# Optimization experiments

Measured on AMD Instinct MI355X. Metric: run time of the kernel, lower is better.

Reference implementation:

```python
import jax, jax.numpy as jnp
import numpy as np

B, N, D_SIM = 4096, 64, 768
NLI_DIM = 768
KK = 5
H1, NUM_CLASSES = 1024, 4


def setup_inputs() -> dict:
    key = jax.random.key(0)
    ks = jax.random.split(key, 8)
    sim_stance_emb = jax.random.normal(ks[0], (B, D_SIM), dtype=jnp.float32)
    nli_stance_emb = jax.random.normal(ks[1], (B, NLI_DIM), dtype=jnp.float32)
    sim_body_emb = jax.random.normal(ks[2], (B, N, D_SIM), dtype=jnp.float32)
    nli_body_emb = jax.random.normal(ks[3], (B, N, NLI_DIM), dtype=jnp.float32)
    fan1 = (KK + 1) * NLI_DIM
    W1 = jax.random.uniform(ks[4], (H1, fan1), jnp.float32, -1.0, 1.0) / jnp.sqrt(fan1)
    b1 = jax.random.uniform(ks[5], (H1,), jnp.float32, -1.0, 1.0) / jnp.sqrt(fan1)
    W2 = jax.random.uniform(ks[6], (NUM_CLASSES, H1), jnp.float32, -1.0, 1.0) / jnp.sqrt(H1)
    b2 = jax.random.uniform(ks[7], (NUM_CLASSES,), jnp.float32, -1.0, 1.0) / jnp.sqrt(H1)
    return {"sim_stance_emb": sim_stance_emb, "nli_stance_emb": nli_stance_emb,
            "sim_body_emb": sim_body_emb, "nli_body_emb": nli_body_emb,
            "W1": W1, "b1": b1, "W2": W2, "b2": b2}


def reference(sim_stance_emb, nli_stance_emb, sim_body_emb, nli_body_emb, W1, b1, W2, b2):
    # sims[b, n] = <sim_stance_emb[b], sim_body_emb[b, n]>  (bmm + squeeze)
    sims = jnp.einsum('bd,bnd->bn', sim_stance_emb, sim_body_emb)
    _, top_idx = jax.lax.top_k(sims, KK)                      # [B, KK]
    # gather top-k nli body sentence embeddings: [B, KK, NLI_DIM]
    top_emb = jnp.take_along_axis(nli_body_emb, top_idx[:, :, None], axis=1)
    xx = jnp.concatenate([nli_stance_emb, top_emb.reshape(top_emb.shape[0], -1)], axis=1)
    xx = jax.nn.relu(xx @ W1.T + b1)
    return xx @ W2.T + b2
```

## Files before the change

### kernel.cpp

```cpp
#include <hip/hip_runtime.h>
#include <stdint.h>
#include <stddef.h>

#define B_N   4096
#define NSENT 64
#define DDIM  768
#define TOPK  5
#define FAN1  4608
#define H1DIM 1024
#define NCLS  4
#define KDIM  4608

typedef __attribute__((ext_vector_type(8))) __bf16 bf16x8;
typedef __attribute__((ext_vector_type(4))) float  f32x4;

__device__ __forceinline__ unsigned short f2bf(float f) {
    unsigned int u = __float_as_uint(f);
    unsigned int r = (u + 0x7fffu + ((u >> 16) & 1u)) >> 16;
    return (unsigned short)r;
}

__device__ __forceinline__ void gl_lds16(const void* g, void* l) {
    __builtin_amdgcn_global_load_lds((__attribute__((address_space(1))) void*)(g),
                                     (__attribute__((address_space(3))) void*)(l),
                                     16, 0, 0);
}

__global__ __launch_bounds__(256) void k_topk_gather(
    const float* __restrict__ sim_stance,
    const float* __restrict__ sim_body,
    const float* __restrict__ nli_stance,
    const float* __restrict__ nli_body,
    unsigned short* __restrict__ xx)
{
    const int b    = blockIdx.x;
    const int tid  = threadIdx.x;
    const int lane = tid & 63;
    const int wave = tid >> 6;
    __shared__ float sims[NSENT];
    __shared__ int   topidx[TOPK];

    const float4* st4 = (const float4*)(sim_stance + (size_t)b * DDIM);
    const float4  s0 = st4[lane], s1 = st4[64 + lane], s2 = st4[128 + lane];

    const float* bodyb = sim_body + (size_t)b * NSENT * DDIM;
    for (int n = wave; n < NSENT; n += 4) {
        const float4* r4 = (const float4*)(bodyb + (size_t)n * DDIM);
        float4 a = r4[lane], c = r4[64 + lane], e = r4[128 + lane];
        float p = a.x*s0.x + a.y*s0.y + a.z*s0.z + a.w*s0.w
                + c.x*s1.x + c.y*s1.y + c.z*s1.z + c.w*s1.w
                + e.x*s2.x + e.y*s2.y + e.z*s2.z + e.w*s2.w;
        #pragma unroll
        for (int off = 32; off; off >>= 1) p += __shfl_xor(p, off);
        if (lane == 0) sims[n] = p;
    }
    __syncthreads();

    if (wave == 0) {
        float v = sims[lane];
        #pragma unroll
        for (int k = 0; k < TOPK; ++k) {
            float bv = v; int bi = lane;
            #pragma unroll
            for (int off = 32; off; off >>= 1) {
                float ov = __shfl_xor(bv, off);
                int   oi = __shfl_xor(bi, off);
                if (ov > bv || (ov == bv && oi < bi)) { bv = ov; bi = oi; }
            }
            if (lane == 0) topidx[k] = bi;
            if (lane == bi) v = -3.402823466e38f;
        }
    }
    __syncthreads();

    unsigned short* xrow = xx + (size_t)b * FAN1;
    if (tid < 192) {
        #pragma unroll
        for (int seg = 0; seg < 6; ++seg) {
            const float* src = (seg == 0)
                ? (nli_stance + (size_t)b * DDIM)
                : (nli_body + ((size_t)b * NSENT + topidx[seg - 1]) * DDIM);
            float4 v = ((const float4*)src)[tid];
            ushort4 o;
            o.x = f2bf(v.x); o.y = f2bf(v.y); o.z = f2bf(v.z); o.w = f2bf(v.w);
            ((ushort4*)(xrow + seg * DDIM))[tid] = o;
        }
    }
}

__global__ __launch_bounds__(256) void k_f32_to_bf16x4(
    const float* __restrict__ in, unsigned short* __restrict__ o, int n4)
{
    int i = blockIdx.x * 256 + threadIdx.x;
    if (i < n4) {
        float4 v = ((const float4*)in)[i];
        ushort4 r;
        r.x = f2bf(v.x); r.y = f2bf(v.y); r.z = f2bf(v.z); r.w = f2bf(v.w);
        ((ushort4*)o)[i] = r;
    }
}

__global__ __launch_bounds__(256, 2) void k_gemm1(
    const unsigned short* __restrict__ A,
    const unsigned short* __restrict__ W,
    const float* __restrict__ bias,
    float* __restrict__ Hd)
{
    constexpr int BM = 128, BN = 64, BK = 32;
    constexpr int K = KDIM;
    __shared__ unsigned short lA[BM * BK];
    __shared__ unsigned short lB[BN * BK];

    const int tid = threadIdx.x, lane = tid & 63, wave = tid >> 6;
    const int bn = blockIdx.x & 15, bm = blockIdx.x >> 4;
    const int wm = wave >> 1, wn = wave & 1;

    const int qA0 = wave * 128 + lane;
    const int qA1 = qA0 + 64;
    const int qB  = wave * 64 + lane;
    const unsigned short* gA0 = A + (size_t)(bm * BM + (qA0 >> 2)) * K + (qA0 & 3) * 8;
    const unsigned short* gA1 = A + (size_t)(bm * BM + (qA1 >> 2)) * K + (qA1 & 3) * 8;
    const unsigned short* gB0 = W + (size_t)(bn * BN + (qB  >> 2)) * K + (qB  & 3) * 8;
    unsigned short* lAd0 = &lA[(wave * 2 + 0) * 512];
    unsigned short* lAd1 = &lA[(wave * 2 + 1) * 512];
    unsigned short* lBd  = &lB[wave * 512];

    const int r16 = lane & 15, kh = (lane >> 4) * 8;
    const unsigned short* pa = &lA[(wm * 64 + r16) * BK + kh];
    const unsigned short* pb = &lB[(wn * 32 + r16) * BK + kh];

    f32x4 acc[4][2];
    #pragma unroll
    for (int m = 0; m < 4; ++m)
        #pragma unroll
        for (int n = 0; n < 2; ++n) acc[m][n] = {0.f, 0.f, 0.f, 0.f};

    for (int kt = 0; kt < K / BK; ++kt) {
        gl_lds16(gA0, lAd0);
        gl_lds16(gA1, lAd1);
        gl_lds16(gB0, lBd);
        gA0 += BK; gA1 += BK; gB0 += BK;
        __syncthreads();

        bf16x8 fa[4], fb[2];
        #pragma unroll
        for (int m = 0; m < 4; ++m) fa[m] = *(const bf16x8*)(pa + m * 16 * BK);
        #pragma unroll
        for (int n = 0; n < 2; ++n) fb[n] = *(const bf16x8*)(pb + n * 16 * BK);
        #pragma unroll
        for (int m = 0; m < 4; ++m)
            #pragma unroll
            for (int n = 0; n < 2; ++n)
                acc[m][n] = __builtin_amdgcn_mfma_f32_16x16x32_bf16(fa[m], fb[n], acc[m][n], 0, 0, 0);
        __syncthreads();
    }

    const int colbase = bn * BN + wn * 32 + r16;
    const int rowbase = bm * BM + wm * 64 + (lane >> 4) * 4;
    #pragma unroll
    for (int n = 0; n < 2; ++n) {
        const int col = colbase + n * 16;
        const float bv = bias[col];
        #pragma unroll
        for (int m = 0; m < 4; ++m) {
            const int row = rowbase + m * 16;
            #pragma unroll
            for (int j = 0; j < 4; ++j) {
                float x = acc[m][n][j] + bv;
                Hd[(size_t)(row + j) * H1DIM + col] = x > 0.f ? x : 0.f;
            }
        }
    }
}

__global__ __launch_bounds__(256) void k_gemm2(
    const float* __restrict__ Hd, const float* __restrict__ W2,
    const float* __restrict__ b2, float* __restrict__ out)
{
    __shared__ float w2s[NCLS * H1DIM];
    const int tid = threadIdx.x, lane = tid & 63, wave = tid >> 6;
    const int row = blockIdx.x * 4 + wave;
    for (int i = tid; i < NCLS * H1DIM; i += 256) w2s[i] = W2[i];
    __syncthreads();

    const float4* h4 = (const float4*)(Hd + (size_t)row * H1DIM);
    const float4* w0 = (const float4*)&w2s[0];
    const float4* w1 = (const float4*)&w2s[H1DIM];
    const float4* w2 = (const float4*)&w2s[2 * H1DIM];
    const float4* w3 = (const float4*)&w2s[3 * H1DIM];
    float a0 = 0.f, a1 = 0.f, a2 = 0.f, a3 = 0.f;
    #pragma unroll
    for (int j = 0; j < 4; ++j) {
        const int idx = j * 64 + lane;
        float4 h = h4[idx], x;
        x = w0[idx]; a0 += h.x*x.x + h.y*x.y + h.z*x.z + h.w*x.w;
        x = w1[idx]; a1 += h.x*x.x + h.y*x.y + h.z*x.z + h.w*x.w;
        x = w2[idx]; a2 += h.x*x.x + h.y*x.y + h.z*x.z + h.w*x.w;
        x = w3[idx]; a3 += h.x*x.x + h.y*x.y + h.z*x.z + h.w*x.w;
    }
    #pragma unroll
    for (int off = 32; off; off >>= 1) {
        a0 += __shfl_xor(a0, off);
        a1 += __shfl_xor(a1, off);
        a2 += __shfl_xor(a2, off);
        a3 += __shfl_xor(a3, off);
    }
    if (lane == 0) {
        float* o = out + (size_t)row * NCLS;
        o[0] = a0 + b2[0]; o[1] = a1 + b2[1]; o[2] = a2 + b2[2]; o[3] = a3 + b2[3];
    }
}

extern "C" void kernel_launch(void* const* d_in, const int* in_sizes, int n_in,
                              void* d_out, int out_size, void* d_ws, size_t ws_size,
                              hipStream_t stream)
{
    const float* sim_stance = (const float*)d_in[0];
    const float* nli_stance = (const float*)d_in[1];
    const float* sim_body   = (const float*)d_in[2];
    const float* nli_body   = (const float*)d_in[3];
    const float* W1 = (const float*)d_in[4];
    const float* b1 = (const float*)d_in[5];
    const float* W2 = (const float*)d_in[6];
    const float* b2 = (const float*)d_in[7];
    float* out = (float*)d_out;

    char* ws = (char*)d_ws;
    unsigned short* xx     = (unsigned short*)ws;
    unsigned short* w1b    = (unsigned short*)(ws + 37748736u);
    float*          hidden = (float*)(ws + 37748736u + 9437184u);

    k_f32_to_bf16x4<<<dim3(4608), dim3(256), 0, stream>>>(W1, w1b, 1179648);
    k_topk_gather<<<dim3(B_N), dim3(256), 0, stream>>>(sim_stance, sim_body,
                                                       nli_stance, nli_body, xx);
    k_gemm1<<<dim3(512), dim3(256), 0, stream>>>(xx, w1b, b1, hidden);
    k_gemm2<<<dim3(1024), dim3(256), 0, stream>>>(hidden, W2, b2, out);
}
```

Baseline: 294.5 us.

## Double GEMM1 K-tile to 64 with XOR-swizzled LDS layout, spread gather over all threads

Raises the GEMM1 K tile from 32 to 64 so each barrier pair covers twice the MFMA work, halving loop iterations and synchronisation overhead. The LDS tile is written with an XOR swizzle on 16-byte chunks, and fragment reads undo it, to avoid LDS bank conflicts now that rows are 128 bytes wide. The top-k gather/convert step now spreads its 1152 float4 tasks across all 256 threads instead of only 192. LDS use per block doubles, which may affect occupancy, and the swizzle indexing adds some address arithmetic.

```diff
diff --git a/kernel.cpp b/kernel.cpp
--- a/kernel.cpp
+++ b/kernel.cpp
@@ -74,17 +74,16 @@
     __syncthreads();
 
     unsigned short* xrow = xx + (size_t)b * FAN1;
-    if (tid < 192) {
-        #pragma unroll
-        for (int seg = 0; seg < 6; ++seg) {
-            const float* src = (seg == 0)
-                ? (nli_stance + (size_t)b * DDIM)
-                : (nli_body + ((size_t)b * NSENT + topidx[seg - 1]) * DDIM);
-            float4 v = ((const float4*)src)[tid];
-            ushort4 o;
-            o.x = f2bf(v.x); o.y = f2bf(v.y); o.z = f2bf(v.z); o.w = f2bf(v.w);
-            ((ushort4*)(xrow + seg * DDIM))[tid] = o;
-        }
+    for (int task = tid; task < 1152; task += 256) {
+        const int seg = task / 192;
+        const int t   = task - seg * 192;
+        const float* src = (seg == 0)
+            ? (nli_stance + (size_t)b * DDIM)
+            : (nli_body + ((size_t)b * NSENT + topidx[seg - 1]) * DDIM);
+        float4 v = ((const float4*)src)[t];
+        ushort4 o;
+        o.x = f2bf(v.x); o.y = f2bf(v.y); o.z = f2bf(v.z); o.w = f2bf(v.w);
+        ((ushort4*)(xrow + seg * DDIM))[t] = o;
     }
 }
 
@@ -106,7 +105,7 @@
     const float* __restrict__ bias,
     float* __restrict__ Hd)
 {
-    constexpr int BM = 128, BN = 64, BK = 32;
+    constexpr int BM = 128, BN = 64, BK = 64;
     constexpr int K = KDIM;
     __shared__ unsigned short lA[BM * BK];
     __shared__ unsigned short lB[BN * BK];
@@ -115,19 +114,30 @@
     const int bn = blockIdx.x & 15, bm = blockIdx.x >> 4;
     const int wm = wave >> 1, wn = wave & 1;
 
-    const int qA0 = wave * 128 + lane;
-    const int qA1 = qA0 + 64;
-    const int qB  = wave * 64 + lane;
-    const unsigned short* gA0 = A + (size_t)(bm * BM + (qA0 >> 2)) * K + (qA0 & 3) * 8;
-    const unsigned short* gA1 = A + (size_t)(bm * BM + (qA1 >> 2)) * K + (qA1 & 3) * 8;
-    const unsigned short* gB0 = W + (size_t)(bn * BN + (qB  >> 2)) * K + (qB  & 3) * 8;
-    unsigned short* lAd0 = &lA[(wave * 2 + 0) * 512];
-    unsigned short* lAd1 = &lA[(wave * 2 + 1) * 512];
-    unsigned short* lBd  = &lB[wave * 512];
-
-    const int r16 = lane & 15, kh = (lane >> 4) * 8;
-    const unsigned short* pa = &lA[(wm * 64 + r16) * BK + kh];
-    const unsigned short* pb = &lB[(wn * 32 + r16) * BK + kh];
+    const int q   = wave * 64 + lane;
+    const int q8  = q >> 3;
+    const int sc  = (q & 7) ^ (q8 & 7);
+    const unsigned short* gA[4];
+    const unsigned short* gB[2];
+    #pragma unroll
+    for (int j = 0; j < 4; ++j)
+        gA[j] = A + (size_t)(bm * BM + j * 32 + q8) * K + sc * 8;
+    #pragma unroll
+    for (int j = 0; j < 2; ++j)
+        gB[j] = W + (size_t)(bn * BN + j * 32 + q8) * K + sc * 8;
+    unsigned short* lAd[4];
+    unsigned short* lBd[2];
+    #pragma unroll
+    for (int j = 0; j < 4; ++j) lAd[j] = &lA[(j * 256 + wave * 64) * 8];
+    #pragma unroll
+    for (int j = 0; j < 2; ++j) lBd[j] = &lB[(j * 256 + wave * 64) * 8];
+
+    const int r16 = lane & 15;
+    const int x   = r16 & 7;
+    const int p0  = (lane >> 4) ^ x;
+    const int p1  = p0 ^ 4;
+    const unsigned short* paBase = &lA[(wm * 64 + r16) * BK];
+    const unsigned short* pbBase = &lB[(wn * 32 + r16) * BK];
 
     f32x4 acc[4][2];
     #pragma unroll
@@ -136,22 +146,31 @@
         for (int n = 0; n < 2; ++n) acc[m][n] = {0.f, 0.f, 0.f, 0.f};
 
     for (int kt = 0; kt < K / BK; ++kt) {
-        gl_lds16(gA0, lAd0);
-        gl_lds16(gA1, lAd1);
-        gl_lds16(gB0, lBd);
-        gA0 += BK; gA1 += BK; gB0 += BK;
+        #pragma unroll
+        for (int j = 0; j < 4; ++j) { gl_lds16(gA[j], lAd[j]); gA[j] += BK; }
+        #pragma unroll
+        for (int j = 0; j < 2; ++j) { gl_lds16(gB[j], lBd[j]); gB[j] += BK; }
         __syncthreads();
 
-        bf16x8 fa[4], fb[2];
-        #pragma unroll
-        for (int m = 0; m < 4; ++m) fa[m] = *(const bf16x8*)(pa + m * 16 * BK);
-        #pragma unroll
-        for (int n = 0; n < 2; ++n) fb[n] = *(const bf16x8*)(pb + n * 16 * BK);
-        #pragma unroll
-        for (int m = 0; m < 4; ++m)
+        bf16x8 fa[4][2], fb[2][2];
+        #pragma unroll
+        for (int m = 0; m < 4; ++m) {
+            fa[m][0] = *(const bf16x8*)(paBase + m * 16 * BK + p0 * 8);
+            fa[m][1] = *(const bf16x8*)(paBase + m * 16 * BK + p1 * 8);
+        }
+        #pragma unroll
+        for (int n = 0; n < 2; ++n) {
+            fb[n][0] = *(const bf16x8*)(pbBase + n * 16 * BK + p0 * 8);
+            fb[n][1] = *(const bf16x8*)(pbBase + n * 16 * BK + p1 * 8);
+        }
+        #pragma unroll
+        for (int h = 0; h < 2; ++h)
             #pragma unroll
-            for (int n = 0; n < 2; ++n)
-                acc[m][n] = __builtin_amdgcn_mfma_f32_16x16x32_bf16(fa[m], fb[n], acc[m][n], 0, 0, 0);
+            for (int m = 0; m < 4; ++m)
+                #pragma unroll
+                for (int n = 0; n < 2; ++n)
+                    acc[m][n] = __builtin_amdgcn_mfma_f32_16x16x32_bf16(
+                        fa[m][h], fb[n][h], acc[m][n], 0, 0, 0);
         __syncthreads();
     }
 
@@ -166,8 +185,8 @@
             const int row = rowbase + m * 16;
             #pragma unroll
             for (int j = 0; j < 4; ++j) {
-                float x = acc[m][n][j] + bv;
-                Hd[(size_t)(row + j) * H1DIM + col] = x > 0.f ? x : 0.f;
+                float v = acc[m][n][j] + bv;
+                Hd[(size_t)(row + j) * H1DIM + col] = v > 0.f ? v : 0.f;
             }
         }
     }
@@ -192,11 +211,11 @@
     #pragma unroll
     for (int j = 0; j < 4; ++j) {
         const int idx = j * 64 + lane;
-        float4 h = h4[idx], x;
-        x = w0[idx]; a0 += h.x*x.x + h.y*x.y + h.z*x.z + h.w*x.w;
-        x = w1[idx]; a1 += h.x*x.x + h.y*x.y + h.z*x.z + h.w*x.w;
-        x = w2[idx]; a2 += h.x*x.x + h.y*x.y + h.z*x.z + h.w*x.w;
-        x = w3[idx]; a3 += h.x*x.x + h.y*x.y + h.z*x.z + h.w*x.w;
+        float4 h = h4[idx], xv;
+        xv = w0[idx]; a0 += h.x*xv.x + h.y*xv.y + h.z*xv.z + h.w*xv.w;
+        xv = w1[idx]; a1 += h.x*xv.x + h.y*xv.y + h.z*xv.z + h.w*xv.w;
+        xv = w2[idx]; a2 += h.x*xv.x + h.y*xv.y + h.z*xv.z + h.w*xv.w;
+        xv = w3[idx]; a3 += h.x*xv.x + h.y*xv.y + h.z*xv.z + h.w*xv.w;
     }
     #pragma unroll
     for (int off = 32; off; off >>= 1) {
```

New measurement: 277.2 us. 5.9% less time.
